# Kernel optimization log

Measured on AMD Instinct MI355X. Metric: run time of the kernel, lower is better.

Reference implementation:

```python
import jax, jax.numpy as jnp
import numpy as np

N_NODES = 6000
DEG = 16
N_EDGES = N_NODES * DEG
D_MODEL = 256
D_MSG = 64
D_FF = 4 * D_MODEL
N_LAYERS = 3
N_SPECIES = 108
RBF_BINS = D_MODEL
RBF_VMIN, RBF_VMAX = 0.0, 8.0


def setup_inputs():
    key = jax.random.key(0)
    ks = jax.random.split(key, 16)
    rng = np.random.default_rng(0)
    # graph: each node i has DEG in-edges (dst block-structured), random sources
    atomic_number = jnp.asarray(rng.integers(1, N_SPECIES, N_NODES), dtype=jnp.int32)
    dst = np.repeat(np.arange(N_NODES), DEG)
    src = rng.integers(0, N_NODES, N_EDGES)
    # angle graph t: nodes = edges of g; edges = all ordered pairs of in-edges sharing dst
    pq = np.array([(p, q) for p in range(DEG) for q in range(DEG) if p != q], dtype=np.int64)
    off = (np.arange(N_NODES) * DEG)[:, None]
    t_src = (off + pq[:, 0][None, :]).reshape(-1)
    t_dst = (off + pq[:, 1][None, :]).reshape(-1)
    r = jax.random.normal(ks[0], (N_EDGES, 3), dtype=jnp.float32) * 2.0  # bond vectors, |r|~3A
    s_dm = 1.0 / np.sqrt(D_MODEL)
    s_dmsg = 1.0 / np.sqrt(D_MSG)
    s_ff = 1.0 / np.sqrt(D_FF)
    return {
        'r': r,
        'atomic_number': atomic_number,
        'src': jnp.asarray(src, dtype=jnp.int32),
        'dst': jnp.asarray(dst, dtype=jnp.int32),
        't_src': jnp.asarray(t_src, dtype=jnp.int32),
        't_dst': jnp.asarray(t_dst, dtype=jnp.int32),
        'emb': jax.random.normal(ks[1], (N_SPECIES, D_MODEL), dtype=jnp.float32),
        'Wsrc': jax.random.normal(ks[2], (N_LAYERS, D_MSG, D_MODEL), dtype=jnp.float32) * s_dm,
        'bsrc': jnp.zeros((N_LAYERS, D_MSG), jnp.float32),
        'Wdst': jax.random.normal(ks[3], (N_LAYERS, D_MSG, D_MODEL), dtype=jnp.float32) * s_dm,
        'bdst': jnp.zeros((N_LAYERS, D_MSG), jnp.float32),
        'Wedge': jax.random.normal(ks[4], (N_LAYERS, D_MSG, D_MODEL), dtype=jnp.float32) * s_dm,
        'bedge': jnp.zeros((N_LAYERS, D_MSG), jnp.float32),
        'attn': jax.random.normal(ks[5], (N_LAYERS, D_MSG), dtype=jnp.float32) * s_dmsg,
        'W1': jax.random.normal(ks[6], (N_LAYERS, D_FF, D_MSG), dtype=jnp.float32) * s_dmsg,
        'b1': jnp.zeros((N_LAYERS, D_FF), jnp.float32),
        'W2': jax.random.normal(ks[7], (N_LAYERS, D_MODEL, D_FF), dtype=jnp.float32) * s_ff,
        'b2': jnp.zeros((N_LAYERS, D_MODEL), jnp.float32),
        'Wfc': jax.random.normal(ks[8], (1, D_MODEL), dtype=jnp.float32) * s_dm,
        'bfc': jnp.zeros((1,), jnp.float32),
    }


def _segment_softmax(logits, seg, num):
    m = jax.ops.segment_max(logits, seg, num_segments=num)
    ex = jnp.exp(logits - m[seg])
    z = jax.ops.segment_sum(ex, seg, num_segments=num)
    return ex / z[seg]


def reference(r, atomic_number, src, dst, t_src, t_dst, emb, Wsrc, bsrc, Wdst, bdst,
              Wedge, bedge, attn, W1, b1, W2, b2, Wfc, bfc):
    x = emb[atomic_number]                                   # [N, d_model]
    d = jnp.linalg.norm(r, axis=1)                           # [E]
    centers = jnp.linspace(RBF_VMIN, RBF_VMAX, RBF_BINS, dtype=r.dtype)
    gamma = 1.0 / (centers[1] - centers[0])
    y = jnp.exp(-gamma * (d[:, None] - centers[None, :]) ** 2)  # [E, d_model]
    rhat = r / d[:, None]
    # cos angle between edge pairs (sign of -r cancels in u_dot_v)
    cos_jik = jnp.clip(jnp.sum(rhat[t_src] * rhat[t_dst], axis=1), -1.0 + 1e-6, 1.0 - 1e-6)
    nch = jnp.arange(D_MSG, dtype=r.dtype)
    z_jik = jnp.cos(nch[None, :] * jnp.arccos(cos_jik)[:, None])  # Chebyshev T_k(cos) [T, 64]
    for l in range(N_LAYERS):
        xj = x @ Wsrc[l].T + bsrc[l]                          # [N, 64]
        xi = x @ Wdst[l].T + bdst[l]
        xij = xj[src] + xi[dst] + (y @ Wedge[l].T + bedge[l])  # [E, 64]
        e_jik = jax.nn.silu(z_jik + xij[t_src] + xij[t_dst])   # [T, 64]
        logits = e_jik @ attn[l]                               # [T]
        a = _segment_softmax(logits, t_dst, N_EDGES)           # edge_softmax over angle graph
        ft = jax.ops.segment_sum(a[:, None] * xij[t_src], t_dst, num_segments=N_EDGES)  # [E, 64]
        xn = jax.ops.segment_sum(ft, dst, num_segments=N_NODES)  # scatter to nodes [N, 64]
        x = jax.nn.silu(xn @ W1[l].T + b1[l]) @ W2[l].T + b2[l]  # FFN -> [N, d_model]
    atomwise = x @ Wfc.T + bfc                                  # [N, 1]
    return jnp.squeeze(jnp.mean(atomwise, axis=0))              # AvgPooling (eV/atom)


if __name__ == '__main__':
    out = reference(**setup_inputs())
    print(out)
```

## Files before the change

### kernel.cpp

```cpp
#include <hip/hip_runtime.h>

#define N_NODES 6000
#define DEG_    16
#define N_EDGES (N_NODES*DEG_)
#define D_MODEL 256
#define D_MSG   64
#define D_FF    1024

#define TBL_N   1024
#define TBL_DMAX 9.0f

typedef __bf16 bf16x8 __attribute__((ext_vector_type(8)));
typedef float floatx4 __attribute__((ext_vector_type(4)));

__device__ __forceinline__ float silu_f(float v) {
    return v * __builtin_amdgcn_rcpf(1.0f + __expf(-v));
}
__device__ __forceinline__ float b2f(unsigned short u) {
    union { unsigned int i; float f; } v; v.i = ((unsigned int)u) << 16; return v.f;
}
__device__ __forceinline__ unsigned short f2b(float f) {
    union { float f; unsigned int i; } v; v.f = f;
    unsigned int r = (v.i + 0x7FFFu + ((v.i >> 16) & 1u)) >> 16;
    return (unsigned short)r;
}

#define EMB4_BLOCKS (N_NODES*D_MODEL/4/256)
#define GEOM_BLOCKS (N_EDGES/256)
#define WPACK1_BLOCKS 96
#define WSDP_BLOCKS 16
__global__ __launch_bounds__(256) void prep_kernel(
    const float* __restrict__ Wsrc, const float* __restrict__ Wdst,
    const float* __restrict__ W1,
    const int* __restrict__ an, const float* __restrict__ emb,
    unsigned short* __restrict__ x,
    const float* __restrict__ r, float* __restrict__ d, float* __restrict__ rhat,
    unsigned short* __restrict__ w1p,
    unsigned short* __restrict__ wsdp) {
    int b = blockIdx.x;
    int t = threadIdx.x;
    if (b < EMB4_BLOCKS) {
        int i4 = b*256 + t;
        int node = i4 >> 6, c4 = i4 & 63;
        float4 v = *(const float4*)(emb + (size_t)an[node]*D_MODEL + c4*4);
        *(ushort4*)(x + (size_t)node*D_MODEL + c4*4) =
            make_ushort4(f2b(v.x), f2b(v.y), f2b(v.z), f2b(v.w));
    } else if (b < EMB4_BLOCKS + GEOM_BLOCKS) {
        int e = (b - EMB4_BLOCKS)*256 + t;
        float xx = r[e*3+0], yy = r[e*3+1], zz = r[e*3+2];
        float n = sqrtf(xx*xx + yy*yy + zz*zz);
        d[e] = n;
        float inv = 1.0f / n;
        *(float4*)(rhat + (size_t)e*4) = make_float4(xx*inv, yy*inv, zz*inv, 0.f);
    } else if (b < EMB4_BLOCKS + GEOM_BLOCKS + WPACK1_BLOCKS) {
        int wb = b - (EMB4_BLOCKS + GEOM_BLOCKS);
        int i2 = wb*256 + t;
        int lp = i2 >> 13;
        int e = i2 & 8191;
        int lane = e & 63, j = (e >> 6) & 1, wv = (e >> 7) & 3, f = e >> 9;
        int row = f*64 + wv*16 + (lane & 15);
        int col = j*32 + (lane >> 4)*8;
        const float* sp = W1 + (size_t)lp*65536 + (size_t)row*64 + col;
        float4 v0 = *(const float4*)sp;
        float4 v1 = *(const float4*)(sp + 4);
        unsigned short h[8] = { f2b(v0.x), f2b(v0.y), f2b(v0.z), f2b(v0.w),
                                f2b(v1.x), f2b(v1.y), f2b(v1.z), f2b(v1.w) };
        *(uint4*)(w1p + (size_t)i2*8) = *(uint4*)h;
    } else {
        int wb = b - (EMB4_BLOCKS + GEOM_BLOCKS + WPACK1_BLOCKS);
        int i = wb*256 + t;
        int lane = i & 63, ks = (i >> 6) & 7, tl = i >> 9;
        int bx = tl >> 2, ns = tl & 3;
        int row = ns*16 + (lane & 15);
        int col = ks*32 + (lane >> 4)*8;
        const float* sp = (bx ? Wdst : Wsrc) + (size_t)row*256 + col;
        float4 v0 = *(const float4*)sp;
        float4 v1 = *(const float4*)(sp + 4);
        unsigned short h[8] = { f2b(v0.x), f2b(v0.y), f2b(v0.z), f2b(v0.w),
                                f2b(v1.x), f2b(v1.y), f2b(v1.z), f2b(v1.w) };
        *(uint4*)(wsdp + (size_t)i*8) = *(uint4*)h;
    }
}

__global__ __launch_bounds__(256) void eplg_kernel(
    const unsigned short* __restrict__ A,
    const unsigned short* __restrict__ wsdp,
    const float* __restrict__ bias1,
    const float* __restrict__ bias2,
    unsigned short* __restrict__ Cg,
    const float* __restrict__ Wsrc, const float* __restrict__ Wdst,
    const float* __restrict__ W2, const float* __restrict__ b2,
    const float* __restrict__ Wfc, const float* __restrict__ bfc,
    unsigned short* __restrict__ wcomb,
    float* __restrict__ bcomb,
    float* __restrict__ wfc2,
    const float* __restrict__ WedgeF,
    const float* __restrict__ bedge,
    float* __restrict__ T,
    float* __restrict__ out) {
    __shared__ __align__(16) unsigned short sm[5120];
    const int t = threadIdx.x;
    const int w = t >> 6, lane = t & 63, lr = lane & 15, lq = lane >> 4;

    if (blockIdx.x < 375) {
        const int m0 = blockIdx.x * 16;
        bf16x8 af[8];
        #pragma unroll
        for (int ks = 0; ks < 8; ++ks)
            af[ks] = *(const bf16x8*)(A + (size_t)(m0 + lr)*256 + ks*32 + lq*8);
        #pragma unroll
        for (int h = 0; h < 2; ++h) {
            int tl = w*2 + h;
            int bx = tl >> 2, ns = tl & 3;
            const unsigned short* pbase = wsdp + ((size_t)tl*512 + lane)*8;
            uint4 pb[8];
            #pragma unroll
            for (int ks = 0; ks < 8; ++ks)
                pb[ks] = *(const uint4*)(pbase + ks*512);
            floatx4 acc = {};
            #pragma unroll
            for (int ks = 0; ks < 8; ++ks)
                acc = __builtin_amdgcn_mfma_f32_16x16x32_bf16(
                    af[ks], *(const bf16x8*)&pb[ks], acc, 0, 0, 0);
            int col = bx*64 + ns*16 + lr;
            float bv = (bx ? bias2 : bias1)[ns*16 + lr];
            #pragma unroll
            for (int rg = 0; rg < 4; ++rg) {
                int gm = m0 + lq*4 + rg;
                Cg[(size_t)gm*128 + col] = f2b(acc[rg] + bv);
            }
        }
        return;
    }
    if (blockIdx.x < 444) {
        int b = blockIdx.x - 375;
        if (b < 64) {
            int lp  = 1 + (b >> 5);
            int wb2 = b & 31;
            const float* W2f = W2 + (size_t)(lp-1)*262144;
            const float* wm[4];
            #pragma unroll
            for (int i = 0; i < 4; ++i) {
                int row = wb2*4 + i;
                wm[i] = (row < 64) ? (Wsrc + (size_t)lp*16384 + row*256)
                                   : (Wdst + (size_t)lp*16384 + (row-64)*256);
            }
            float acc[4][4] = {};
            int c0 = t*4;
            #pragma unroll 8
            for (int c = 0; c < 256; ++c) {
                float4 w2v = *(const float4*)(W2f + (size_t)c*1024 + c0);
                #pragma unroll
                for (int i = 0; i < 4; ++i) {
                    float wv2 = wm[i][c];
                    acc[i][0] = fmaf(wv2, w2v.x, acc[i][0]);
                    acc[i][1] = fmaf(wv2, w2v.y, acc[i][1]);
                    acc[i][2] = fmaf(wv2, w2v.z, acc[i][2]);
                    acc[i][3] = fmaf(wv2, w2v.w, acc[i][3]);
                }
            }
            int fc = t >> 4, j = (t >> 3) & 1, lq2 = (t >> 1) & 3, cpos = (t & 1) * 4;
            #pragma unroll
            for (int i = 0; i < 4; ++i) {
                int row = wb2*4 + i;
                int wv2 = row >> 5, ns = (row >> 4) & 1, lr2 = row & 15;
                *(ushort4*)(wcomb + (size_t)(lp-1)*131072
                            + (size_t)fc*8192 + wv2*2048 + ns*1024 + j*512 + (lq2*16+lr2)*8 + cpos) =
                    make_ushort4(f2b(acc[i][0]), f2b(acc[i][1]), f2b(acc[i][2]), f2b(acc[i][3]));
            }
        } else if (b < 68) {
            int c = (b - 64)*256 + t;
            const float* W2f = W2 + 2*262144;
            float a[8] = {};
            #pragma unroll 4
            for (int k = 0; k < 256; k += 8) {
                #pragma unroll
                for (int j = 0; j < 8; ++j)
                    a[j] = fmaf(Wfc[k+j], W2f[(size_t)(k+j)*1024 + c], a[j]);
            }
            wfc2[c] = ((a[0]+a[1]) + (a[2]+a[3])) + ((a[4]+a[5]) + (a[6]+a[7]));
        } else {
            int lp = 1 + (t >> 7);
            int row = t & 127;
            const float* b2l = b2 + (lp-1)*256;
            const float* wmrow = (row < 64) ? (Wsrc + (size_t)lp*16384 + row*256)
                                            : (Wdst + (size_t)lp*16384 + (row-64)*256);
            float acc = 0.f;
            #pragma unroll 8
            for (int c = 0; c < 256; ++c) acc += wmrow[c] * b2l[c];
            acc += (row < 64) ? bias1[lp*64 + row] : bias2[lp*64 + (row-64)];
            bcomb[(lp-1)*128 + row] = acc;
            if (t == 0) {
                float bo = 0.f;
                const float* b23 = b2 + 2*256;
                #pragma unroll 8
                for (int c = 0; c < 256; ++c) bo += Wfc[c] * b23[c];
                out[0] = bo + bfc[0];
            }
        }
        return;
    }
    {
        int b = blockIdx.x - 444;
        float* s_rbf = (float*)sm;
        const int rl = t >> 5;
        const int row = b*8 + rl;
        const int cg = t & 31;
        const float gamma = 31.875f;
        const float step  = 8.0f / 255.0f;
        const float step_t = TBL_DMAX / (float)(TBL_N - 1);
        float dv = (float)row * step_t;
        {
            int k0 = cg*8;
            #pragma unroll
            for (int j = 0; j < 8; ++j) {
                float x2 = dv - (float)(k0+j)*step;
                s_rbf[rl*260 + k0 + j] = __expf(-gamma*x2*x2);
            }
        }
        __syncthreads();
        const float* rb = s_rbf + rl*260;
        #pragma unroll
        for (int c = 0; c < 6; ++c) {
            int col = cg*6 + c;
            const float* wr = WedgeF + (size_t)col*256;
            float a0 = 0.f, a1 = 0.f, a2 = 0.f, a3 = 0.f;
            #pragma unroll 4
            for (int k = 0; k < 256; k += 4) {
                float4 wv = *(const float4*)(wr + k);
                a0 = fmaf(rb[k+0], wv.x, a0);
                a1 = fmaf(rb[k+1], wv.y, a1);
                a2 = fmaf(rb[k+2], wv.z, a2);
                a3 = fmaf(rb[k+3], wv.w, a3);
            }
            T[(size_t)row*192 + col] = bedge[col] + (a0 + a1) + (a2 + a3);
        }
    }
}

#define HP 72
#define CP2 136
__global__ __launch_bounds__(256) void ffw_kernel(
    const unsigned short* __restrict__ XN,
    const unsigned short* __restrict__ W1p,
    const float* __restrict__ b1l,
    const unsigned short* __restrict__ WCp,
    const float* __restrict__ bcl,
    unsigned short* __restrict__ XO,
    int M) {
    __shared__ __align__(16) unsigned short s_h[16*HP];
    __shared__ __align__(16) unsigned short s_c[16*CP2];
    const int t = threadIdx.x;
    const int wv = t >> 6, lane = t & 63, lr = lane & 15, lq = lane >> 4;
    const int m0 = blockIdx.x * 16;

    int ga = m0 + lr;
    bool aok = ga < M;
    uint4 a0 = aok ? *(const uint4*)(XN + (size_t)ga*64 + lq*8) : make_uint4(0,0,0,0);
    uint4 a1 = aok ? *(const uint4*)(XN + (size_t)ga*64 + 32 + lq*8) : make_uint4(0,0,0,0);

    floatx4 acc2[2] = {};

    const unsigned short* W1b = W1p + (size_t)wv*1024 + lane*8;
    const unsigned short* WCb = WCp + (size_t)wv*2048 + lane*8;

    uint4 pb1[2], pb2[4];
    pb1[0] = *(const uint4*)(W1b);
    pb1[1] = *(const uint4*)(W1b + 512);
    pb2[0] = *(const uint4*)(WCb);
    pb2[1] = *(const uint4*)(WCb + 512);
    pb2[2] = *(const uint4*)(WCb + 1024);
    pb2[3] = *(const uint4*)(WCb + 1536);

    for (int f = 0; f < 16; ++f) {
        uint4 cb1_0 = pb1[0], cb1_1 = pb1[1];
        uint4 cb2_0 = pb2[0], cb2_1 = pb2[1], cb2_2 = pb2[2], cb2_3 = pb2[3];
        float bv1 = b1l[f*64 + wv*16 + lr];
        if (f < 15) {
            const unsigned short* n1 = W1b + (f+1)*4096;
            const unsigned short* n2 = WCb + (f+1)*8192;
            pb1[0] = *(const uint4*)(n1);
            pb1[1] = *(const uint4*)(n1 + 512);
            pb2[0] = *(const uint4*)(n2);
            pb2[1] = *(const uint4*)(n2 + 512);
            pb2[2] = *(const uint4*)(n2 + 1024);
            pb2[3] = *(const uint4*)(n2 + 1536);
        }
        floatx4 hacc = {};
        hacc = __builtin_amdgcn_mfma_f32_16x16x32_bf16(
            *(const bf16x8*)&a0, *(const bf16x8*)&cb1_0, hacc, 0,0,0);
        hacc = __builtin_amdgcn_mfma_f32_16x16x32_bf16(
            *(const bf16x8*)&a1, *(const bf16x8*)&cb1_1, hacc, 0,0,0);
        {
            int col = wv*16 + lr;
            #pragma unroll
            for (int rg = 0; rg < 4; ++rg) {
                int row = lq*4 + rg;
                s_h[row*HP + col] = f2b(silu_f(hacc[rg] + bv1));
            }
        }
        __syncthreads();
        bf16x8 ha0 = *(const bf16x8*)(&s_h[lr*HP + lq*8]);
        bf16x8 ha1 = *(const bf16x8*)(&s_h[lr*HP + 32 + lq*8]);
        acc2[0] = __builtin_amdgcn_mfma_f32_16x16x32_bf16(ha0, *(const bf16x8*)&cb2_0, acc2[0], 0,0,0);
        acc2[0] = __builtin_amdgcn_mfma_f32_16x16x32_bf16(ha1, *(const bf16x8*)&cb2_1, acc2[0], 0,0,0);
        acc2[1] = __builtin_amdgcn_mfma_f32_16x16x32_bf16(ha0, *(const bf16x8*)&cb2_2, acc2[1], 0,0,0);
        acc2[1] = __builtin_amdgcn_mfma_f32_16x16x32_bf16(ha1, *(const bf16x8*)&cb2_3, acc2[1], 0,0,0);
        __syncthreads();
    }

    #pragma unroll
    for (int ns = 0; ns < 2; ++ns) {
        int col = wv*32 + ns*16 + lr;
        float bv = bcl[col];
        #pragma unroll
        for (int rg = 0; rg < 4; ++rg) {
            int row = lq*4 + rg;
            s_c[row*CP2 + col] = f2b(acc2[ns][rg] + bv);
        }
    }
    __syncthreads();
    {
        int row = t >> 4, c8 = t & 15;
        int gm = m0 + row;
        if (gm < M)
            *(uint4*)(XO + (size_t)gm*128 + c8*8) = *(const uint4*)(s_c + row*CP2 + c8*8);
    }
}

__global__ __launch_bounds__(256) void ffa_kernel(
    const unsigned short* __restrict__ XN,
    const unsigned short* __restrict__ W1p,
    const float* __restrict__ b1l,
    const float* __restrict__ wfc2,
    float* __restrict__ out, int M) {
    __shared__ float red[256];
    const int t = threadIdx.x;
    const int wv = t >> 6, lane = t & 63, lr = lane & 15, lq = lane >> 4;
    const int m0 = blockIdx.x * 16;

    int ga = m0 + lr;
    bool aok = ga < M;
    uint4 a0 = aok ? *(const uint4*)(XN + (size_t)ga*64 + lq*8) : make_uint4(0,0,0,0);
    uint4 a1 = aok ? *(const uint4*)(XN + (size_t)ga*64 + 32 + lq*8) : make_uint4(0,0,0,0);

    const unsigned short* W1b = W1p + (size_t)wv*1024 + lane*8;
    uint4 pb0 = *(const uint4*)(W1b);
    uint4 pb1 = *(const uint4*)(W1b + 512);

    float partial = 0.f;
    for (int f = 0; f < 16; ++f) {
        uint4 c0 = pb0, c1 = pb1;
        if (f < 15) {
            pb0 = *(const uint4*)(W1b + (f+1)*4096);
            pb1 = *(const uint4*)(W1b + (f+1)*4096 + 512);
        }
        floatx4 hacc = {};
        hacc = __builtin_amdgcn_mfma_f32_16x16x32_bf16(
            *(const bf16x8*)&a0, *(const bf16x8*)&c0, hacc, 0,0,0);
        hacc = __builtin_amdgcn_mfma_f32_16x16x32_bf16(
            *(const bf16x8*)&a1, *(const bf16x8*)&c1, hacc, 0,0,0);
        float bv1 = b1l[f*64 + wv*16 + lr];
        float wvv = wfc2[f*64 + wv*16 + lr];
        #pragma unroll
        for (int rg = 0; rg < 4; ++rg) {
            int gm = m0 + lq*4 + rg;
            if (gm < M) partial += silu_f(hacc[rg] + bv1) * wvv;
        }
    }
    red[t] = partial;
    __syncthreads();
    for (int off = 128; off > 0; off >>= 1) {
        if (t < off) red[t] += red[t+off];
        __syncthreads();
    }
    if (t == 0) atomicAdd(out, red[0] * (1.0f/(float)N_NODES));
}

__global__ __launch_bounds__(256) void angle_kernel(
    const unsigned short* __restrict__ xjxi,
    const float* __restrict__ T,
    int lc0,
    const float* __restrict__ dvec,
    const float* __restrict__ rhat,
    const int*   __restrict__ src,
    const float* __restrict__ attn,
    unsigned short* __restrict__ xn) {
    __shared__ __align__(16) float s_xij[16][68];
    __shared__ float s_rhat[16][4];
    __shared__ float s_logit[16][17];
    __shared__ float s_a[16][17];
    __shared__ float s_w[16];
    const int tt = threadIdx.x;
    const int node = blockIdx.x;

    if (tt < 16) {
        float4 rv = *(const float4*)(rhat + (size_t)(node*DEG_ + tt)*4);
        s_rhat[tt][0] = rv.x; s_rhat[tt][1] = rv.y; s_rhat[tt][2] = rv.z; s_rhat[tt][3] = 0.f;
        s_logit[tt][tt] = -1e30f;
    }
    {
        int p = tt >> 4, c4 = tt & 15;
        int e = node*DEG_ + p;
        int se = src[e];
        ushort4 aj = *(const ushort4*)(xjxi + (size_t)se*128 + c4*4);
        ushort4 ai = *(const ushort4*)(xjxi + (size_t)node*128 + 64 + c4*4);
        const float inv_step_t = (float)(TBL_N - 1) / TBL_DMAX;
        float u = fminf(dvec[e] * inv_step_t, (float)(TBL_N - 2) + 0.999f);
        int i0 = (int)u;
        float fr = u - (float)i0;
        const float* t0 = T + (size_t)i0*192 + lc0 + c4*4;
        float4 v0 = *(const float4*)t0;
        float4 v1 = *(const float4*)(t0 + 192);
        s_xij[p][c4*4+0] = b2f(aj.x) + b2f(ai.x) + fmaf(fr, v1.x - v0.x, v0.x);
        s_xij[p][c4*4+1] = b2f(aj.y) + b2f(ai.y) + fmaf(fr, v1.y - v0.y, v0.y);
        s_xij[p][c4*4+2] = b2f(aj.z) + b2f(ai.z) + fmaf(fr, v1.z - v0.z, v0.z);
        s_xij[p][c4*4+3] = b2f(aj.w) + b2f(ai.w) + fmaf(fr, v1.w - v0.w, v0.w);
    }
    __syncthreads();
    int pp = 0, qq = 0;
    float lg = 0.f;
    if (tt < 240) {
        int pair = tt >> 1, half = tt & 1;
        pp = (int)((1.0f + sqrtf(8.0f*(float)pair + 1.0f)) * 0.5f);
        qq = pair - ((pp*(pp-1)) >> 1);
        float c = s_rhat[pp][0]*s_rhat[qq][0] + s_rhat[pp][1]*s_rhat[qq][1]
                + s_rhat[pp][2]*s_rhat[qq][2];
        c = fminf(fmaxf(c, -0.999999f), 0.999999f);
        float c2 = 2.0f * c;
        float tk0, tk1;
        if (half) {
            float T2  = fmaf(c2, c, -1.0f);
            float T3  = fmaf(2.0f*T2,  c,   -c);
            float T4  = fmaf(2.0f*T2,  T2,  -1.0f);
            float T7  = fmaf(2.0f*T4,  T3,  -c);
            float T8  = fmaf(2.0f*T4,  T4,  -1.0f);
            float T15 = fmaf(2.0f*T8,  T7,  -c);
            float T16 = fmaf(2.0f*T8,  T8,  -1.0f);
            float T31 = fmaf(2.0f*T16, T15, -c);
            float T32 = fmaf(2.0f*T16, T16, -1.0f);
            float T33 = fmaf(2.0f*T32, c,   -T31);
            tk0 = T32; tk1 = T33;
        } else {
            tk0 = 1.0f; tk1 = c;
        }
        const float* xp = &s_xij[pp][0] + half*32;
        const float* xq = &s_xij[qq][0] + half*32;
        const float* at = attn + half*32;
        float acc = 0.f;
        #pragma unroll
        for (int k0 = 0; k0 < 32; k0 += 4) {
            float4 xp4 = *(const float4*)(xp + k0);
            float4 xq4 = *(const float4*)(xq + k0);
            float a0 = at[k0+0], a1 = at[k0+1], a2 = at[k0+2], a3 = at[k0+3];
            float v0 = tk0 + xp4.x + xq4.x;
            acc = fmaf(a0, silu_f(v0), acc);
            { float tn2 = c2*tk1 - tk0; tk0 = tk1; tk1 = tn2; }
            float v1 = tk0 + xp4.y + xq4.y;
            acc = fmaf(a1, silu_f(v1), acc);
            { float tn2 = c2*tk1 - tk0; tk0 = tk1; tk1 = tn2; }
            float v2 = tk0 + xp4.z + xq4.z;
            acc = fmaf(a2, silu_f(v2), acc);
            { float tn2 = c2*tk1 - tk0; tk0 = tk1; tk1 = tn2; }
            float v3 = tk0 + xp4.w + xq4.w;
            acc = fmaf(a3, silu_f(v3), acc);
            { float tn2 = c2*tk1 - tk0; tk0 = tk1; tk1 = tn2; }
        }
        lg = acc;
    }
    lg += __shfl_xor(lg, 1);
    if (tt < 240 && (tt & 1) == 0) {
        s_logit[pp][qq] = lg;
        s_logit[qq][pp] = lg;
    }
    __syncthreads();
    {
        int q = tt >> 4, p = tt & 15;
        float l = s_logit[p][q];
        float m = l;
        m = fmaxf(m, __shfl_xor(m, 1));
        m = fmaxf(m, __shfl_xor(m, 2));
        m = fmaxf(m, __shfl_xor(m, 4));
        m = fmaxf(m, __shfl_xor(m, 8));
        float e = __expf(l - m);
        float z = e;
        z += __shfl_xor(z, 1);
        z += __shfl_xor(z, 2);
        z += __shfl_xor(z, 4);
        z += __shfl_xor(z, 8);
        s_a[p][q] = e * __builtin_amdgcn_rcpf(z);
    }
    __syncthreads();
    {
        int p = tt >> 4, q = tt & 15;
        float a = s_a[p][q];
        a += __shfl_xor(a, 1);
        a += __shfl_xor(a, 2);
        a += __shfl_xor(a, 4);
        a += __shfl_xor(a, 8);
        if (q == 0) s_w[p] = a;
    }
    __syncthreads();
    if (tt < 64) {
        float acc = 0.f;
        #pragma unroll
        for (int p = 0; p < 16; ++p) acc += s_w[p] * s_xij[p][tt];
        xn[(size_t)node*64 + tt] = f2b(acc);
    }
}

extern "C" void kernel_launch(void* const* d_in, const int* in_sizes, int n_in,
                              void* d_out, int out_size, void* d_ws, size_t ws_size,
                              hipStream_t stream) {
    (void)in_sizes; (void)n_in; (void)out_size; (void)ws_size;
    const float* r    = (const float*)d_in[0];
    const int*   an   = (const int*)  d_in[1];
    const int*   src  = (const int*)  d_in[2];
    const float* emb  = (const float*)d_in[6];
    const float* Wsrc = (const float*)d_in[7];
    const float* bsrc = (const float*)d_in[8];
    const float* Wdst = (const float*)d_in[9];
    const float* bdst = (const float*)d_in[10];
    const float* Wedge= (const float*)d_in[11];
    const float* bedge= (const float*)d_in[12];
    const float* attn = (const float*)d_in[13];
    const float* W1   = (const float*)d_in[14];
    const float* b1   = (const float*)d_in[15];
    const float* W2   = (const float*)d_in[16];
    const float* b2   = (const float*)d_in[17];
    const float* Wfc  = (const float*)d_in[18];
    const float* bfc  = (const float*)d_in[19];

    char* ws = (char*)d_ws;
    float* d_d              = (float*)(ws);
    float* d_rhat           = (float*)(ws + 384000);
    unsigned short* d_wsdp  = (unsigned short*)(ws + 1920000);
    unsigned short* d_x     = (unsigned short*)(ws + 4180992);
    unsigned short* d_xjxi  = (unsigned short*)(ws + 7252992);
    float* d_table          = (float*)(ws + 8788992);
    unsigned short* d_xn    = (unsigned short*)(ws + 45652992);
    unsigned short* d_wcomb = (unsigned short*)(ws + 46420992);
    float* d_bcomb          = (float*)(ws + 46945280);
    float* d_wfc2           = (float*)(ws + 46946304);
    unsigned short* d_w1p   = (unsigned short*)(ws + 47048704);
    float* out = (float*)d_out;

    prep_kernel<<<EMB4_BLOCKS + GEOM_BLOCKS + WPACK1_BLOCKS + WSDP_BLOCKS,
                  256, 0, stream>>>(
        Wsrc, Wdst, W1, an, emb, d_x, r, d_d, d_rhat, d_w1p, d_wsdp);

    eplg_kernel<<<375 + 69 + 128, 256, 0, stream>>>(
        d_x, d_wsdp, bsrc, bdst, d_xjxi,
        Wsrc, Wdst, W2, b2, Wfc, bfc,
        d_wcomb, d_bcomb, d_wfc2,
        Wedge, bedge, d_table, out);

    angle_kernel<<<N_NODES, 256, 0, stream>>>(
        d_xjxi, d_table, 0, d_d, d_rhat, src, attn, d_xn);
    ffw_kernel<<<375, 256, 0, stream>>>(
        d_xn, d_w1p, b1, d_wcomb, d_bcomb, d_xjxi, N_NODES);

    angle_kernel<<<N_NODES, 256, 0, stream>>>(
        d_xjxi, d_table, 64, d_d, d_rhat, src, attn + 64, d_xn);
    ffw_kernel<<<375, 256, 0, stream>>>(
        d_xn, d_w1p + 65536, b1 + 1024, d_wcomb + 131072, d_bcomb + 128, d_xjxi, N_NODES);

    angle_kernel<<<N_NODES, 256, 0, stream>>>(
        d_xjxi, d_table, 128, d_d, d_rhat, src, attn + 128, d_xn);
    ffa_kernel<<<375, 256, 0, stream>>>(
        d_xn, d_w1p + 131072, b1 + 2048, d_wfc2, out, N_NODES);
}
```

Measured before the change: 244.7 us.

## Split eplg kernel, move table to prep and weight folding into angle kernel

Removes the mixed eplg kernel. The RBF edge table build now runs in prep_kernel and is stored as bf16 instead of fp32, which halves table traffic in the angle kernels. The layer-0 node GEMM becomes a standalone gemm0_kernel. The W2-fused weight and bias precomputation runs as 69 extra blocks appended to the first angle_kernel launch, so it overlaps with angle work. The bf16 table adds rounding error to the interpolated edge features.

```diff
diff --git a/kernel.cpp b/kernel.cpp
--- a/kernel.cpp
+++ b/kernel.cpp
@@ -29,6 +29,7 @@
 #define GEOM_BLOCKS (N_EDGES/256)
 #define WPACK1_BLOCKS 96
 #define WSDP_BLOCKS 16
+#define TBL_BLOCKS 128
 __global__ __launch_bounds__(256) void prep_kernel(
     const float* __restrict__ Wsrc, const float* __restrict__ Wdst,
     const float* __restrict__ W1,
@@ -36,7 +37,11 @@
     unsigned short* __restrict__ x,
     const float* __restrict__ r, float* __restrict__ d, float* __restrict__ rhat,
     unsigned short* __restrict__ w1p,
-    unsigned short* __restrict__ wsdp) {
+    unsigned short* __restrict__ wsdp,
+    const float* __restrict__ WedgeF,
+    const float* __restrict__ bedge,
+    unsigned short* __restrict__ T) {
+    __shared__ float s_rbf[8*260];
     int b = blockIdx.x;
     int t = threadIdx.x;
     if (b < EMB4_BLOCKS) {
@@ -66,7 +71,7 @@
         unsigned short h[8] = { f2b(v0.x), f2b(v0.y), f2b(v0.z), f2b(v0.w),
                                 f2b(v1.x), f2b(v1.y), f2b(v1.z), f2b(v1.w) };
         *(uint4*)(w1p + (size_t)i2*8) = *(uint4*)h;
-    } else {
+    } else if (b < EMB4_BLOCKS + GEOM_BLOCKS + WPACK1_BLOCKS + WSDP_BLOCKS) {
         int wb = b - (EMB4_BLOCKS + GEOM_BLOCKS + WPACK1_BLOCKS);
         int i = wb*256 + t;
         int lane = i & 63, ks = (i >> 6) & 7, tl = i >> 9;
@@ -79,132 +84,10 @@
         unsigned short h[8] = { f2b(v0.x), f2b(v0.y), f2b(v0.z), f2b(v0.w),
                                 f2b(v1.x), f2b(v1.y), f2b(v1.z), f2b(v1.w) };
         *(uint4*)(wsdp + (size_t)i*8) = *(uint4*)h;
-    }
-}
-
-__global__ __launch_bounds__(256) void eplg_kernel(
-    const unsigned short* __restrict__ A,
-    const unsigned short* __restrict__ wsdp,
-    const float* __restrict__ bias1,
-    const float* __restrict__ bias2,
-    unsigned short* __restrict__ Cg,
-    const float* __restrict__ Wsrc, const float* __restrict__ Wdst,
-    const float* __restrict__ W2, const float* __restrict__ b2,
-    const float* __restrict__ Wfc, const float* __restrict__ bfc,
-    unsigned short* __restrict__ wcomb,
-    float* __restrict__ bcomb,
-    float* __restrict__ wfc2,
-    const float* __restrict__ WedgeF,
-    const float* __restrict__ bedge,
-    float* __restrict__ T,
-    float* __restrict__ out) {
-    __shared__ __align__(16) unsigned short sm[5120];
-    const int t = threadIdx.x;
-    const int w = t >> 6, lane = t & 63, lr = lane & 15, lq = lane >> 4;
-
-    if (blockIdx.x < 375) {
-        const int m0 = blockIdx.x * 16;
-        bf16x8 af[8];
-        #pragma unroll
-        for (int ks = 0; ks < 8; ++ks)
-            af[ks] = *(const bf16x8*)(A + (size_t)(m0 + lr)*256 + ks*32 + lq*8);
-        #pragma unroll
-        for (int h = 0; h < 2; ++h) {
-            int tl = w*2 + h;
-            int bx = tl >> 2, ns = tl & 3;
-            const unsigned short* pbase = wsdp + ((size_t)tl*512 + lane)*8;
-            uint4 pb[8];
-            #pragma unroll
-            for (int ks = 0; ks < 8; ++ks)
-                pb[ks] = *(const uint4*)(pbase + ks*512);
-            floatx4 acc = {};
-            #pragma unroll
-            for (int ks = 0; ks < 8; ++ks)
-                acc = __builtin_amdgcn_mfma_f32_16x16x32_bf16(
-                    af[ks], *(const bf16x8*)&pb[ks], acc, 0, 0, 0);
-            int col = bx*64 + ns*16 + lr;
-            float bv = (bx ? bias2 : bias1)[ns*16 + lr];
-            #pragma unroll
-            for (int rg = 0; rg < 4; ++rg) {
-                int gm = m0 + lq*4 + rg;
-                Cg[(size_t)gm*128 + col] = f2b(acc[rg] + bv);
-            }
-        }
-        return;
-    }
-    if (blockIdx.x < 444) {
-        int b = blockIdx.x - 375;
-        if (b < 64) {
-            int lp  = 1 + (b >> 5);
-            int wb2 = b & 31;
-            const float* W2f = W2 + (size_t)(lp-1)*262144;
-            const float* wm[4];
-            #pragma unroll
-            for (int i = 0; i < 4; ++i) {
-                int row = wb2*4 + i;
-                wm[i] = (row < 64) ? (Wsrc + (size_t)lp*16384 + row*256)
-                                   : (Wdst + (size_t)lp*16384 + (row-64)*256);
-            }
-            float acc[4][4] = {};
-            int c0 = t*4;
-            #pragma unroll 8
-            for (int c = 0; c < 256; ++c) {
-                float4 w2v = *(const float4*)(W2f + (size_t)c*1024 + c0);
-                #pragma unroll
-                for (int i = 0; i < 4; ++i) {
-                    float wv2 = wm[i][c];
-                    acc[i][0] = fmaf(wv2, w2v.x, acc[i][0]);
-                    acc[i][1] = fmaf(wv2, w2v.y, acc[i][1]);
-                    acc[i][2] = fmaf(wv2, w2v.z, acc[i][2]);
-                    acc[i][3] = fmaf(wv2, w2v.w, acc[i][3]);
-                }
-            }
-            int fc = t >> 4, j = (t >> 3) & 1, lq2 = (t >> 1) & 3, cpos = (t & 1) * 4;
-            #pragma unroll
-            for (int i = 0; i < 4; ++i) {
-                int row = wb2*4 + i;
-                int wv2 = row >> 5, ns = (row >> 4) & 1, lr2 = row & 15;
-                *(ushort4*)(wcomb + (size_t)(lp-1)*131072
-                            + (size_t)fc*8192 + wv2*2048 + ns*1024 + j*512 + (lq2*16+lr2)*8 + cpos) =
-                    make_ushort4(f2b(acc[i][0]), f2b(acc[i][1]), f2b(acc[i][2]), f2b(acc[i][3]));
-            }
-        } else if (b < 68) {
-            int c = (b - 64)*256 + t;
-            const float* W2f = W2 + 2*262144;
-            float a[8] = {};
-            #pragma unroll 4
-            for (int k = 0; k < 256; k += 8) {
-                #pragma unroll
-                for (int j = 0; j < 8; ++j)
-                    a[j] = fmaf(Wfc[k+j], W2f[(size_t)(k+j)*1024 + c], a[j]);
-            }
-            wfc2[c] = ((a[0]+a[1]) + (a[2]+a[3])) + ((a[4]+a[5]) + (a[6]+a[7]));
-        } else {
-            int lp = 1 + (t >> 7);
-            int row = t & 127;
-            const float* b2l = b2 + (lp-1)*256;
-            const float* wmrow = (row < 64) ? (Wsrc + (size_t)lp*16384 + row*256)
-                                            : (Wdst + (size_t)lp*16384 + (row-64)*256);
-            float acc = 0.f;
-            #pragma unroll 8
-            for (int c = 0; c < 256; ++c) acc += wmrow[c] * b2l[c];
-            acc += (row < 64) ? bias1[lp*64 + row] : bias2[lp*64 + (row-64)];
-            bcomb[(lp-1)*128 + row] = acc;
-            if (t == 0) {
-                float bo = 0.f;
-                const float* b23 = b2 + 2*256;
-                #pragma unroll 8
-                for (int c = 0; c < 256; ++c) bo += Wfc[c] * b23[c];
-                out[0] = bo + bfc[0];
-            }
-        }
-        return;
-    }
-    {
-        int b = blockIdx.x - 444;
-        float* s_rbf = (float*)sm;
+    } else {
+        int bb = b - (EMB4_BLOCKS + GEOM_BLOCKS + WPACK1_BLOCKS + WSDP_BLOCKS);
         const int rl = t >> 5;
-        const int row = b*8 + rl;
+        const int row = bb*8 + rl;
         const int cg = t & 31;
         const float gamma = 31.875f;
         const float step  = 8.0f / 255.0f;
@@ -233,7 +116,44 @@
                 a2 = fmaf(rb[k+2], wv.z, a2);
                 a3 = fmaf(rb[k+3], wv.w, a3);
             }
-            T[(size_t)row*192 + col] = bedge[col] + (a0 + a1) + (a2 + a3);
+            T[(size_t)row*192 + col] = f2b(bedge[col] + (a0 + a1) + (a2 + a3));
+        }
+    }
+}
+
+__global__ __launch_bounds__(256) void gemm0_kernel(
+    const unsigned short* __restrict__ A,
+    const unsigned short* __restrict__ wsdp,
+    const float* __restrict__ bias1,
+    const float* __restrict__ bias2,
+    unsigned short* __restrict__ Cg) {
+    const int t = threadIdx.x;
+    const int w = t >> 6, lane = t & 63, lr = lane & 15, lq = lane >> 4;
+    const int m0 = blockIdx.x * 16;
+    bf16x8 af[8];
+    #pragma unroll
+    for (int ks = 0; ks < 8; ++ks)
+        af[ks] = *(const bf16x8*)(A + (size_t)(m0 + lr)*256 + ks*32 + lq*8);
+    #pragma unroll
+    for (int h = 0; h < 2; ++h) {
+        int tl = w*2 + h;
+        int bx = tl >> 2, ns = tl & 3;
+        const unsigned short* pbase = wsdp + ((size_t)tl*512 + lane)*8;
+        uint4 pb[8];
+        #pragma unroll
+        for (int ks = 0; ks < 8; ++ks)
+            pb[ks] = *(const uint4*)(pbase + ks*512);
+        floatx4 acc = {};
+        #pragma unroll
+        for (int ks = 0; ks < 8; ++ks)
+            acc = __builtin_amdgcn_mfma_f32_16x16x32_bf16(
+                af[ks], *(const bf16x8*)&pb[ks], acc, 0, 0, 0);
+        int col = bx*64 + ns*16 + lr;
+        float bv = (bx ? bias2 : bias1)[ns*16 + lr];
+        #pragma unroll
+        for (int rg = 0; rg < 4; ++rg) {
+            int gm = m0 + lq*4 + rg;
+            Cg[(size_t)gm*128 + col] = f2b(acc[rg] + bv);
         }
     }
 }
@@ -379,21 +299,99 @@
 
 __global__ __launch_bounds__(256) void angle_kernel(
     const unsigned short* __restrict__ xjxi,
-    const float* __restrict__ T,
+    const unsigned short* __restrict__ T,
     int lc0,
     const float* __restrict__ dvec,
     const float* __restrict__ rhat,
     const int*   __restrict__ src,
     const float* __restrict__ attn,
-    unsigned short* __restrict__ xn) {
+    unsigned short* __restrict__ xn,
+    const float* __restrict__ Wsrc, const float* __restrict__ Wdst,
+    const float* __restrict__ W2, const float* __restrict__ b2,
+    const float* __restrict__ Wfc, const float* __restrict__ bfc,
+    const float* __restrict__ bsrc, const float* __restrict__ bdst,
+    unsigned short* __restrict__ wcomb,
+    float* __restrict__ bcomb,
+    float* __restrict__ wfc2,
+    float* __restrict__ out) {
     __shared__ __align__(16) float s_xij[16][68];
     __shared__ float s_rhat[16][4];
     __shared__ float s_logit[16][17];
     __shared__ float s_a[16][17];
     __shared__ float s_w[16];
     const int tt = threadIdx.x;
+
+    if (blockIdx.x >= N_NODES) {
+        int b = blockIdx.x - N_NODES;
+        int t = tt;
+        if (b < 64) {
+            int lp  = 1 + (b >> 5);
+            int wb2 = b & 31;
+            const float* W2f = W2 + (size_t)(lp-1)*262144;
+            const float* wm[4];
+            #pragma unroll
+            for (int i = 0; i < 4; ++i) {
+                int row = wb2*4 + i;
+                wm[i] = (row < 64) ? (Wsrc + (size_t)lp*16384 + row*256)
+                                   : (Wdst + (size_t)lp*16384 + (row-64)*256);
+            }
+            float acc[4][4] = {};
+            int c0 = t*4;
+            #pragma unroll 8
+            for (int c = 0; c < 256; ++c) {
+                float4 w2v = *(const float4*)(W2f + (size_t)c*1024 + c0);
+                #pragma unroll
+                for (int i = 0; i < 4; ++i) {
+                    float wv2 = wm[i][c];
+                    acc[i][0] = fmaf(wv2, w2v.x, acc[i][0]);
+                    acc[i][1] = fmaf(wv2, w2v.y, acc[i][1]);
+                    acc[i][2] = fmaf(wv2, w2v.z, acc[i][2]);
+                    acc[i][3] = fmaf(wv2, w2v.w, acc[i][3]);
+                }
+            }
+            int fc = t >> 4, j = (t >> 3) & 1, lq2 = (t >> 1) & 3, cpos = (t & 1) * 4;
+            #pragma unroll
+            for (int i = 0; i < 4; ++i) {
+                int row = wb2*4 + i;
+                int wv2 = row >> 5, ns = (row >> 4) & 1, lr2 = row & 15;
+                *(ushort4*)(wcomb + (size_t)(lp-1)*131072
+                            + (size_t)fc*8192 + wv2*2048 + ns*1024 + j*512 + (lq2*16+lr2)*8 + cpos) =
+                    make_ushort4(f2b(acc[i][0]), f2b(acc[i][1]), f2b(acc[i][2]), f2b(acc[i][3]));
+            }
+        } else if (b < 68) {
+            int c = (b - 64)*256 + t;
+            const float* W2f = W2 + 2*262144;
+            float a[8] = {};
+            #pragma unroll 4
+            for (int k = 0; k < 256; k += 8) {
+                #pragma unroll
+                for (int j = 0; j < 8; ++j)
+                    a[j] = fmaf(Wfc[k+j], W2f[(size_t)(k+j)*1024 + c], a[j]);
+            }
+            wfc2[c] = ((a[0]+a[1]) + (a[2]+a[3])) + ((a[4]+a[5]) + (a[6]+a[7]));
+        } else {
+            int lp = 1 + (t >> 7);
+            int row = t & 127;
+            const float* b2l = b2 + (lp-1)*256;
+            const float* wmrow = (row < 64) ? (Wsrc + (size_t)lp*16384 + row*256)
+                                            : (Wdst + (size_t)lp*16384 + (row-64)*256);
+            float acc = 0.f;
+            #pragma unroll 8
+            for (int c = 0; c < 256; ++c) acc += wmrow[c] * b2l[c];
+            acc += (row < 64) ? bsrc[lp*64 + row] : bdst[lp*64 + (row-64)];
+            bcomb[(lp-1)*128 + row] = acc;
+            if (t == 0) {
+                float bo = 0.f;
+                const float* b23 = b2 + 2*256;
+                #pragma unroll 8
+                for (int c = 0; c < 256; ++c) bo += Wfc[c] * b23[c];
+                out[0] = bo + bfc[0];
+            }
+        }
+        return;
+    }
+
     const int node = blockIdx.x;
-
     if (tt < 16) {
         float4 rv = *(const float4*)(rhat + (size_t)(node*DEG_ + tt)*4);
         s_rhat[tt][0] = rv.x; s_rhat[tt][1] = rv.y; s_rhat[tt][2] = rv.z; s_rhat[tt][3] = 0.f;
@@ -409,13 +407,14 @@
         float u = fminf(dvec[e] * inv_step_t, (float)(TBL_N - 2) + 0.999f);
         int i0 = (int)u;
         float fr = u - (float)i0;
-        const float* t0 = T + (size_t)i0*192 + lc0 + c4*4;
-        float4 v0 = *(const float4*)t0;
-        float4 v1 = *(const float4*)(t0 + 192);
-        s_xij[p][c4*4+0] = b2f(aj.x) + b2f(ai.x) + fmaf(fr, v1.x - v0.x, v0.x);
-        s_xij[p][c4*4+1] = b2f(aj.y) + b2f(ai.y) + fmaf(fr, v1.y - v0.y, v0.y);
-        s_xij[p][c4*4+2] = b2f(aj.z) + b2f(ai.z) + fmaf(fr, v1.z - v0.z, v0.z);
-        s_xij[p][c4*4+3] = b2f(aj.w) + b2f(ai.w) + fmaf(fr, v1.w - v0.w, v0.w);
+        const unsigned short* t0 = T + (size_t)i0*192 + lc0 + c4*4;
+        ushort4 w0 = *(const ushort4*)t0;
+        ushort4 w1 = *(const ushort4*)(t0 + 192);
+        float v0x = b2f(w0.x), v0y = b2f(w0.y), v0z = b2f(w0.z), v0w = b2f(w0.w);
+        s_xij[p][c4*4+0] = b2f(aj.x) + b2f(ai.x) + fmaf(fr, b2f(w1.x) - v0x, v0x);
+        s_xij[p][c4*4+1] = b2f(aj.y) + b2f(ai.y) + fmaf(fr, b2f(w1.y) - v0y, v0y);
+        s_xij[p][c4*4+2] = b2f(aj.z) + b2f(ai.z) + fmaf(fr, b2f(w1.z) - v0z, v0z);
+        s_xij[p][c4*4+3] = b2f(aj.w) + b2f(ai.w) + fmaf(fr, b2f(w1.w) - v0w, v0w);
     }
     __syncthreads();
     int pp = 0, qq = 0;
@@ -537,7 +536,7 @@
     unsigned short* d_wsdp  = (unsigned short*)(ws + 1920000);
     unsigned short* d_x     = (unsigned short*)(ws + 4180992);
     unsigned short* d_xjxi  = (unsigned short*)(ws + 7252992);
-    float* d_table          = (float*)(ws + 8788992);
+    unsigned short* d_table = (unsigned short*)(ws + 8788992);
     unsigned short* d_xn    = (unsigned short*)(ws + 45652992);
     unsigned short* d_wcomb = (unsigned short*)(ws + 46420992);
     float* d_bcomb          = (float*)(ws + 46945280);
@@ -545,28 +544,31 @@
     unsigned short* d_w1p   = (unsigned short*)(ws + 47048704);
     float* out = (float*)d_out;
 
-    prep_kernel<<<EMB4_BLOCKS + GEOM_BLOCKS + WPACK1_BLOCKS + WSDP_BLOCKS,
+    prep_kernel<<<EMB4_BLOCKS + GEOM_BLOCKS + WPACK1_BLOCKS + WSDP_BLOCKS + TBL_BLOCKS,
                   256, 0, stream>>>(
-        Wsrc, Wdst, W1, an, emb, d_x, r, d_d, d_rhat, d_w1p, d_wsdp);
-
-    eplg_kernel<<<375 + 69 + 128, 256, 0, stream>>>(
-        d_x, d_wsdp, bsrc, bdst, d_xjxi,
-        Wsrc, Wdst, W2, b2, Wfc, bfc,
-        d_wcomb, d_bcomb, d_wfc2,
-        Wedge, bedge, d_table, out);
-
-    angle_kernel<<<N_NODES, 256, 0, stream>>>(
-        d_xjxi, d_table, 0, d_d, d_rhat, src, attn, d_xn);
+        Wsrc, Wdst, W1, an, emb, d_x, r, d_d, d_rhat, d_w1p, d_wsdp,
+        Wedge, bedge, d_table);
+
+    gemm0_kernel<<<375, 256, 0, stream>>>(d_x, d_wsdp, bsrc, bdst, d_xjxi);
+
+    angle_kernel<<<N_NODES + 69, 256, 0, stream>>>(
+        d_xjxi, d_table, 0, d_d, d_rhat, src, attn, d_xn,
+        Wsrc, Wdst, W2, b2, Wfc, bfc, bsrc, bdst,
+        d_wcomb, d_bcomb, d_wfc2, out);
     ffw_kernel<<<375, 256, 0, stream>>>(
         d_xn, d_w1p, b1, d_wcomb, d_bcomb, d_xjxi, N_NODES);
 
     angle_kernel<<<N_NODES, 256, 0, stream>>>(
-        d_xjxi, d_table, 64, d_d, d_rhat, src, attn + 64, d_xn);
+        d_xjxi, d_table, 64, d_d, d_rhat, src, attn + 64, d_xn,
+        Wsrc, Wdst, W2, b2, Wfc, bfc, bsrc, bdst,
+        d_wcomb, d_bcomb, d_wfc2, out);
     ffw_kernel<<<375, 256, 0, stream>>>(
         d_xn, d_w1p + 65536, b1 + 1024, d_wcomb + 131072, d_bcomb + 128, d_xjxi, N_NODES);
 
     angle_kernel<<<N_NODES, 256, 0, stream>>>(
-        d_xjxi, d_table, 128, d_d, d_rhat, src, attn + 128, d_xn);
+        d_xjxi, d_table, 128, d_d, d_rhat, src, attn + 128, d_xn,
+        Wsrc, Wdst, W2, b2, Wfc, bfc, bsrc, bdst,
+        d_wcomb, d_bcomb, d_wfc2, out);
     ffa_kernel<<<375, 256, 0, stream>>>(
         d_xn, d_w1p + 131072, b1 + 2048, d_wfc2, out, N_NODES);
 }
```

After: 338.7 us. 1.38x slower.

## Build RBF edge table with bf16 MFMA and store it as bf16

Applied to the files above, without the earlier changes.

The edge-feature lookup table (RBF expansion times Wedge, 1024 distance points by 192 columns) is now computed with bf16 MFMA tiles instead of scalar fp32 FMAs over shared memory. Wedge is prepacked into MFMA fragment layout in the prep kernel. The table is stored in bf16, which halves its footprint and the gather traffic in the three angle kernels, and the table part of the grid drops from 128 blocks to 16. The cost is lower precision in both the RBF basis and the interpolated edge term.

```diff
diff --git a/kernel.cpp b/kernel.cpp
--- a/kernel.cpp
+++ b/kernel.cpp
@@ -29,14 +29,16 @@
 #define GEOM_BLOCKS (N_EDGES/256)
 #define WPACK1_BLOCKS 96
 #define WSDP_BLOCKS 16
+#define WPACKE_BLOCKS 24
 __global__ __launch_bounds__(256) void prep_kernel(
     const float* __restrict__ Wsrc, const float* __restrict__ Wdst,
-    const float* __restrict__ W1,
+    const float* __restrict__ W1, const float* __restrict__ Wedge,
     const int* __restrict__ an, const float* __restrict__ emb,
     unsigned short* __restrict__ x,
     const float* __restrict__ r, float* __restrict__ d, float* __restrict__ rhat,
     unsigned short* __restrict__ w1p,
-    unsigned short* __restrict__ wsdp) {
+    unsigned short* __restrict__ wsdp,
+    unsigned short* __restrict__ wedgep) {
     int b = blockIdx.x;
     int t = threadIdx.x;
     if (b < EMB4_BLOCKS) {
@@ -66,7 +68,7 @@
         unsigned short h[8] = { f2b(v0.x), f2b(v0.y), f2b(v0.z), f2b(v0.w),
                                 f2b(v1.x), f2b(v1.y), f2b(v1.z), f2b(v1.w) };
         *(uint4*)(w1p + (size_t)i2*8) = *(uint4*)h;
-    } else {
+    } else if (b < EMB4_BLOCKS + GEOM_BLOCKS + WPACK1_BLOCKS + WSDP_BLOCKS) {
         int wb = b - (EMB4_BLOCKS + GEOM_BLOCKS + WPACK1_BLOCKS);
         int i = wb*256 + t;
         int lane = i & 63, ks = (i >> 6) & 7, tl = i >> 9;
@@ -79,6 +81,19 @@
         unsigned short h[8] = { f2b(v0.x), f2b(v0.y), f2b(v0.z), f2b(v0.w),
                                 f2b(v1.x), f2b(v1.y), f2b(v1.z), f2b(v1.w) };
         *(uint4*)(wsdp + (size_t)i*8) = *(uint4*)h;
+    } else {
+        int wb = b - (EMB4_BLOCKS + GEOM_BLOCKS + WPACK1_BLOCKS + WSDP_BLOCKS);
+        int i = wb*256 + t;
+        int lane = i & 63, ks = (i >> 6) & 7, rem = i >> 9;
+        int ns = rem % 3, w = rem / 3;
+        int row = 48*w + ns*16 + (lane & 15);
+        int col = ks*32 + (lane >> 4)*8;
+        const float* sp = Wedge + (size_t)row*256 + col;
+        float4 v0 = *(const float4*)sp;
+        float4 v1 = *(const float4*)(sp + 4);
+        unsigned short h[8] = { f2b(v0.x), f2b(v0.y), f2b(v0.z), f2b(v0.w),
+                                f2b(v1.x), f2b(v1.y), f2b(v1.z), f2b(v1.w) };
+        *(uint4*)(wedgep + (size_t)i*8) = *(uint4*)h;
     }
 }
 
@@ -94,11 +109,10 @@
     unsigned short* __restrict__ wcomb,
     float* __restrict__ bcomb,
     float* __restrict__ wfc2,
-    const float* __restrict__ WedgeF,
+    const unsigned short* __restrict__ Bwp,
     const float* __restrict__ bedge,
-    float* __restrict__ T,
+    unsigned short* __restrict__ T,
     float* __restrict__ out) {
-    __shared__ __align__(16) unsigned short sm[5120];
     const int t = threadIdx.x;
     const int w = t >> 6, lane = t & 63, lr = lane & 15, lq = lane >> 4;
 
@@ -201,39 +215,43 @@
         return;
     }
     {
-        int b = blockIdx.x - 444;
-        float* s_rbf = (float*)sm;
-        const int rl = t >> 5;
-        const int row = b*8 + rl;
-        const int cg = t & 31;
+        const int m0t = (blockIdx.x - 444) * 64;
         const float gamma = 31.875f;
         const float step  = 8.0f / 255.0f;
         const float step_t = TBL_DMAX / (float)(TBL_N - 1);
-        float dv = (float)row * step_t;
-        {
-            int k0 = cg*8;
+        float dv = (float)(m0t + w*16 + lr) * step_t;
+        bf16x8 af[8];
+        #pragma unroll
+        for (int ks = 0; ks < 8; ++ks) {
+            unsigned short h[8];
+            int kb = ks*32 + lq*8;
             #pragma unroll
             for (int j = 0; j < 8; ++j) {
-                float x2 = dv - (float)(k0+j)*step;
-                s_rbf[rl*260 + k0 + j] = __expf(-gamma*x2*x2);
-            }
-        }
-        __syncthreads();
-        const float* rb = s_rbf + rl*260;
-        #pragma unroll
-        for (int c = 0; c < 6; ++c) {
-            int col = cg*6 + c;
-            const float* wr = WedgeF + (size_t)col*256;
-            float a0 = 0.f, a1 = 0.f, a2 = 0.f, a3 = 0.f;
-            #pragma unroll 4
-            for (int k = 0; k < 256; k += 4) {
-                float4 wv = *(const float4*)(wr + k);
-                a0 = fmaf(rb[k+0], wv.x, a0);
-                a1 = fmaf(rb[k+1], wv.y, a1);
-                a2 = fmaf(rb[k+2], wv.z, a2);
-                a3 = fmaf(rb[k+3], wv.w, a3);
-            }
-            T[(size_t)row*192 + col] = bedge[col] + (a0 + a1) + (a2 + a3);
+                float tt2 = dv - (float)(kb+j)*step;
+                h[j] = f2b(__expf(-gamma*tt2*tt2));
+            }
+            af[ks] = *(bf16x8*)h;
+        }
+        const unsigned short* Bl = Bwp + lane*8;
+        #pragma unroll
+        for (int ct = 0; ct < 12; ++ct) {
+            const unsigned short* Bb = Bl + (ct/3)*12288 + (ct%3)*4096;
+            uint4 pb[8];
+            #pragma unroll
+            for (int ks = 0; ks < 8; ++ks)
+                pb[ks] = *(const uint4*)(Bb + ks*512);
+            floatx4 acc = {};
+            #pragma unroll
+            for (int ks = 0; ks < 8; ++ks)
+                acc = __builtin_amdgcn_mfma_f32_16x16x32_bf16(
+                    af[ks], *(const bf16x8*)&pb[ks], acc, 0, 0, 0);
+            int bc = (ct/3)*48 + (ct%3)*16 + lr;
+            float bv = bedge[bc];
+            #pragma unroll
+            for (int rg = 0; rg < 4; ++rg) {
+                int row = m0t + w*16 + lq*4 + rg;
+                T[(size_t)row*192 + bc] = f2b(acc[rg] + bv);
+            }
         }
     }
 }
@@ -379,7 +397,7 @@
 
 __global__ __launch_bounds__(256) void angle_kernel(
     const unsigned short* __restrict__ xjxi,
-    const float* __restrict__ T,
+    const unsigned short* __restrict__ T,
     int lc0,
     const float* __restrict__ dvec,
     const float* __restrict__ rhat,
@@ -409,13 +427,14 @@
         float u = fminf(dvec[e] * inv_step_t, (float)(TBL_N - 2) + 0.999f);
         int i0 = (int)u;
         float fr = u - (float)i0;
-        const float* t0 = T + (size_t)i0*192 + lc0 + c4*4;
-        float4 v0 = *(const float4*)t0;
-        float4 v1 = *(const float4*)(t0 + 192);
-        s_xij[p][c4*4+0] = b2f(aj.x) + b2f(ai.x) + fmaf(fr, v1.x - v0.x, v0.x);
-        s_xij[p][c4*4+1] = b2f(aj.y) + b2f(ai.y) + fmaf(fr, v1.y - v0.y, v0.y);
-        s_xij[p][c4*4+2] = b2f(aj.z) + b2f(ai.z) + fmaf(fr, v1.z - v0.z, v0.z);
-        s_xij[p][c4*4+3] = b2f(aj.w) + b2f(ai.w) + fmaf(fr, v1.w - v0.w, v0.w);
+        const unsigned short* t0 = T + (size_t)i0*192 + lc0 + c4*4;
+        ushort4 w0 = *(const ushort4*)t0;
+        ushort4 w1 = *(const ushort4*)(t0 + 192);
+        float v0x = b2f(w0.x), v0y = b2f(w0.y), v0z = b2f(w0.z), v0w = b2f(w0.w);
+        s_xij[p][c4*4+0] = b2f(aj.x) + b2f(ai.x) + fmaf(fr, b2f(w1.x) - v0x, v0x);
+        s_xij[p][c4*4+1] = b2f(aj.y) + b2f(ai.y) + fmaf(fr, b2f(w1.y) - v0y, v0y);
+        s_xij[p][c4*4+2] = b2f(aj.z) + b2f(ai.z) + fmaf(fr, b2f(w1.z) - v0z, v0z);
+        s_xij[p][c4*4+3] = b2f(aj.w) + b2f(ai.w) + fmaf(fr, b2f(w1.w) - v0w, v0w);
     }
     __syncthreads();
     int pp = 0, qq = 0;
@@ -535,9 +554,10 @@
     float* d_d              = (float*)(ws);
     float* d_rhat           = (float*)(ws + 384000);
     unsigned short* d_wsdp  = (unsigned short*)(ws + 1920000);
+    unsigned short* d_wedgep= (unsigned short*)(ws + 1985536);
     unsigned short* d_x     = (unsigned short*)(ws + 4180992);
     unsigned short* d_xjxi  = (unsigned short*)(ws + 7252992);
-    float* d_table          = (float*)(ws + 8788992);
+    unsigned short* d_table = (unsigned short*)(ws + 8788992);
     unsigned short* d_xn    = (unsigned short*)(ws + 45652992);
     unsigned short* d_wcomb = (unsigned short*)(ws + 46420992);
     float* d_bcomb          = (float*)(ws + 46945280);
@@ -545,15 +565,15 @@
     unsigned short* d_w1p   = (unsigned short*)(ws + 47048704);
     float* out = (float*)d_out;
 
-    prep_kernel<<<EMB4_BLOCKS + GEOM_BLOCKS + WPACK1_BLOCKS + WSDP_BLOCKS,
+    prep_kernel<<<EMB4_BLOCKS + GEOM_BLOCKS + WPACK1_BLOCKS + WSDP_BLOCKS + WPACKE_BLOCKS,
                   256, 0, stream>>>(
-        Wsrc, Wdst, W1, an, emb, d_x, r, d_d, d_rhat, d_w1p, d_wsdp);
-
-    eplg_kernel<<<375 + 69 + 128, 256, 0, stream>>>(
+        Wsrc, Wdst, W1, Wedge, an, emb, d_x, r, d_d, d_rhat, d_w1p, d_wsdp, d_wedgep);
+
+    eplg_kernel<<<375 + 69 + 16, 256, 0, stream>>>(
         d_x, d_wsdp, bsrc, bdst, d_xjxi,
         Wsrc, Wdst, W2, b2, Wfc, bfc,
         d_wcomb, d_bcomb, d_wfc2,
-        Wedge, bedge, d_table, out);
+        d_wedgep, bedge, d_table, out);
 
     angle_kernel<<<N_NODES, 256, 0, stream>>>(
         d_xjxi, d_table, 0, d_d, d_rhat, src, attn, d_xn);
```

Result: faster. 220.0 us (-10.1%).
